# Performance work log

Hardware: AMD Instinct MI355X
Metric: run time of the kernel (lower is better)

Reference implementation:

```python
import jax, jax.numpy as jnp
import numpy as np

EMBED_DIM = 128
TEMP_DIM = EMBED_DIM // 4  # 32
NUM_TYPES = 50
DATE_SCALE = 1825.0
LN_EPS = 1e-5


def _layernorm(x, w, b):
    m = jnp.mean(x, axis=-1, keepdims=True)
    v = jnp.mean((x - m) ** 2, axis=-1, keepdims=True)
    return (x - m) * jax.lax.rsqrt(v + LN_EPS) * w + b


def setup_inputs() -> dict:
    key = jax.random.key(0)
    ks = jax.random.split(key, 16)
    B, L = 4096, 200
    inp = {
        "treatment_ids": jax.random.randint(ks[0], (B, L), 0, NUM_TYPES, dtype=jnp.int64 if jax.config.jax_enable_x64 else jnp.int32),
        "dates": jax.random.uniform(ks[1], (B, L), dtype=jnp.float32) * DATE_SCALE,
        "lengths": jax.random.randint(ks[2], (B,), 0, L + 1, dtype=jnp.int32),
        # parameters
        "emb": jax.random.normal(ks[3], (NUM_TYPES, EMBED_DIM), jnp.float32),
        "tp_w": jax.random.normal(ks[4], (1, TEMP_DIM), jnp.float32) * 0.1,
        "tp_b": jnp.zeros((TEMP_DIM,), jnp.float32),
        "tp_lnw": jnp.ones((TEMP_DIM,), jnp.float32),
        "tp_lnb": jnp.zeros((TEMP_DIM,), jnp.float32),
        "w1": jax.random.normal(ks[5], (EMBED_DIM + TEMP_DIM, EMBED_DIM), jnp.float32) * 0.05,
        "b1": jnp.zeros((EMBED_DIM,), jnp.float32),
        "ln1w": jnp.ones((EMBED_DIM,), jnp.float32),
        "ln1b": jnp.zeros((EMBED_DIM,), jnp.float32),
        "w2": jax.random.normal(ks[6], (EMBED_DIM, EMBED_DIM), jnp.float32) * 0.05,
        "b2": jnp.zeros((EMBED_DIM,), jnp.float32),
        "ln2w": jnp.ones((EMBED_DIM,), jnp.float32),
        "ln2b": jnp.zeros((EMBED_DIM,), jnp.float32),
    }
    return inp


def reference(treatment_ids, dates, lengths, emb, tp_w, tp_b, tp_lnw, tp_lnb,
              w1, b1, ln1w, ln1b, w2, b2, ln2w, ln2b):
    B, L = treatment_ids.shape
    mask = (jnp.arange(L)[None, :] < lengths[:, None]).astype(dates.dtype)  # [B, L]

    # embedding lookup [B, L, D]
    treat = emb[treatment_ids]

    # temporal projection: Linear(1 -> D/4) + LN + GELU
    dn = (dates / DATE_SCALE)[..., None]                      # [B, L, 1]
    temporal = dn * tp_w[0] + tp_b                            # [B, L, D/4]
    temporal = jax.nn.gelu(_layernorm(temporal, tp_lnw, tp_lnb), approximate=False)

    combined = jnp.concatenate([treat, temporal], axis=-1)    # [B, L, D + D/4]

    # sequence encoder (dropout is identity at eval)
    h = jnp.einsum("blk,kd->bld", combined, w1) + b1
    h = jax.nn.gelu(_layernorm(h, ln1w, ln1b), approximate=False)
    h = jnp.einsum("blk,kd->bld", h, w2) + b2
    h = _layernorm(h, ln2w, ln2b)                             # [B, L, D]

    # masked mean pool; empty histories -> zeros
    counts = jnp.sum(mask, axis=1, keepdims=True)             # [B, 1]
    pooled = jnp.sum(h * mask[..., None], axis=1) / jnp.maximum(counts, 1.0)
    return jnp.where(counts > 0, pooled, 0.0)                 # [B, D]
```

## Files before the change

kernel.cpp:

```cpp
#include <hip/hip_runtime.h>
#include <cmath>

#define LN_EPS 1e-5f

typedef float  f32x4  __attribute__((ext_vector_type(4)));
typedef short  short8 __attribute__((ext_vector_type(8)));
typedef unsigned int uint4v __attribute__((ext_vector_type(4)));

#define W1F_U4 2560
#define W2F_U4 2048
#define WLDS_U4 4608

__device__ __forceinline__ unsigned short f32_bf16_rne(float f) {
    union { float f; unsigned u; } v; v.f = f;
    unsigned r = v.u + 0x7FFFu + ((v.u >> 16) & 1u);
    return (unsigned short)(r >> 16);
}

__device__ __forceinline__ unsigned cvt_pk_bf16(float lo, float hi) {
    unsigned r;
    asm("v_cvt_pk_bf16_f32 %0, %1, %2" : "=v"(r) : "v"(lo), "v"(hi));
    return r;
}

__device__ __forceinline__ float gelu_f(float x) {
    float ax = fabsf(x);
    float a  = ax * 0.70710678118654752f;
    float t  = __builtin_amdgcn_rcpf(fmaf(0.3275911f, a, 1.0f));
    float p  = t * fmaf(t, fmaf(t, fmaf(t, fmaf(t, 1.061405429f, -1.453152027f),
                                        1.421413741f), -0.284496736f), 0.254829592f);
    float e  = __builtin_amdgcn_exp2f(-1.44269504089f * a * a);
    float E  = fmaf(-p, e, 1.0f);
    return 0.5f * fmaf(ax, E, x);
}

template<int C>
__device__ __forceinline__ float dpp_radd(float x) {
    int t = __builtin_amdgcn_update_dpp(0, __builtin_bit_cast(int, x), C, 0xF, 0xF, true);
    return x + __builtin_bit_cast(float, t);
}
__device__ __forceinline__ float red16(float x) {
    x = dpp_radd<0x128>(x);
    x = dpp_radd<0x124>(x);
    x = dpp_radd<0x122>(x);
    x = dpp_radd<0x121>(x);
    return x;
}

__global__ void prep_kernel(const float* __restrict__ w1, const float* __restrict__ w2,
                            const float* __restrict__ emb,
                            const float* __restrict__ tp_w, const float* __restrict__ tp_b,
                            unsigned* __restrict__ ws, int emb_pairs) {
    const int tid = blockIdx.x * 256 + threadIdx.x;
    uint4v* w1f = (uint4v*)ws;
    uint4v* w2f = w1f + W1F_U4;
    unsigned* emb16 = (unsigned*)(w2f + W2F_U4);

    for (int i = tid; i < W1F_U4; i += 8192) {
        const int lane = i & 63, nt = (i >> 6) & 7, kt = i >> 9;
        const int k0 = kt * 32 + (lane >> 4) * 8, n = nt * 16 + (lane & 15);
        uint4v r;
        #pragma unroll
        for (int j2 = 0; j2 < 4; ++j2) {
            unsigned lo = f32_bf16_rne(w1[(k0 + 2 * j2) * 128 + n]);
            unsigned hi = f32_bf16_rne(w1[(k0 + 2 * j2 + 1) * 128 + n]);
            r[j2] = lo | (hi << 16);
        }
        w1f[i] = r;
    }
    for (int i = tid; i < W2F_U4; i += 8192) {
        const int lane = i & 63, nt = (i >> 6) & 7, kt = i >> 9;
        const int k0 = kt * 32 + (lane >> 4) * 8, n = nt * 16 + (lane & 15);
        uint4v r;
        #pragma unroll
        for (int j2 = 0; j2 < 4; ++j2) {
            unsigned lo = f32_bf16_rne(w2[(k0 + 2 * j2) * 128 + n]);
            unsigned hi = f32_bf16_rne(w2[(k0 + 2 * j2 + 1) * 128 + n]);
            r[j2] = lo | (hi << 16);
        }
        w2f[i] = r;
    }
    for (int i = tid; i < emb_pairs; i += 8192) {
        unsigned lo = f32_bf16_rne(emb[2 * i]);
        unsigned hi = f32_bf16_rne(emb[2 * i + 1]);
        emb16[i] = lo | (hi << 16);
    }
    if (tid == 0) {
        float Sw = 0.f, Sb = 0.f, Sww = 0.f, Swb = 0.f, Sbb = 0.f;
        for (int j = 0; j < 32; ++j) {
            const float ww = tp_w[j], bb = tp_b[j];
            Sw += ww; Sb += bb; Sww += ww * ww; Swb += ww * bb; Sbb += bb * bb;
        }
        float* tps = (float*)(emb16 + emb_pairs);
        tps[0] = Sw; tps[1] = Sb; tps[2] = Sww; tps[3] = Swb; tps[4] = Sbb;
    }
}

__global__ __launch_bounds__(768, 3) void encoder_mfma(
    const int*   __restrict__ tids,  const float* __restrict__ dates,
    const int*   __restrict__ lengths,
    const float* __restrict__ tp_w,  const float* __restrict__ tp_b,
    const float* __restrict__ tp_lnw,const float* __restrict__ tp_lnb,
    const float* __restrict__ b1,    const float* __restrict__ ln1w, const float* __restrict__ ln1b,
    const float* __restrict__ b2,    const float* __restrict__ ln2w, const float* __restrict__ ln2b,
    const unsigned* __restrict__ ws, float* __restrict__ out,
    int B, int L, int emb_pairs)
{
    __shared__ __align__(16) uint4v wlds[WLDS_U4];
    __shared__ __align__(16) unsigned short a2[12][4][64][8];
    __shared__ float poolbuf[3][4][128];
    __shared__ __align__(16) f32x4 tcoef[32];
    __shared__ __align__(16) f32x4 ecoef1[128];
    __shared__ __align__(16) f32x4 ecoef2[128];

    const int tid = threadIdx.x;
    const int lane = tid & 63, w = tid >> 6;
    const int c = lane & 15, g = lane >> 4;
    const int row = w >> 2, wr = w & 3;
    const int b   = blockIdx.x * 3 + row;

    #pragma unroll
    for (int i = 0; i < 6; ++i)
        wlds[i * 768 + tid] = ((const uint4v*)ws)[i * 768 + tid];

    const unsigned short* emb16 = (const unsigned short*)((const uint4v*)ws + W1F_U4 + W2F_U4);
    const float* tps = (const float*)(emb16 + emb_pairs * 2);

    if (tid < 32)  tcoef[tid]  = (f32x4){tp_w[tid], tp_b[tid], tp_lnw[tid], tp_lnb[tid]};
    if (tid < 128) {
        ecoef1[tid] = (f32x4){b1[tid], ln1w[tid], ln1b[tid], 0.f};
        ecoef2[tid] = (f32x4){b2[tid], ln2w[tid], ln2b[tid], 0.f};
    }
    __syncthreads();

    const float Sw = tps[0], Sb = tps[1], Sww = tps[2], Swb = tps[3], Sbb = tps[4];

    const int len = (b < B) ? min(max(lengths[b], 0), L) : 0;
    const int ntiles = (len + 15) >> 4;

    float pool[8];
    #pragma unroll
    for (int nt = 0; nt < 8; ++nt) pool[nt] = 0.f;
    const int srl = lane ^ ((lane >> 3) & 3);

    for (int t = wr; t < ntiles; t += 4) {
        const int R0 = t << 4;
        const int pc = min(R0 + c, L - 1);
        const int id = tids[b * L + pc];
        const float d = dates[b * L + pc] * (1.f / 1825.f);

        short8 tfrag;
        {
            const float tm = fmaf(d, Sw, Sb) * (1.f / 32.f);
            float tv = fmaf(d * d, Sww, fmaf(2.f * d, Swb, Sbb)) * (1.f / 32.f) - tm * tm;
            const float trs = rsqrtf(fmaxf(tv, 0.f) + LN_EPS);
            const int j0 = g * 8;
            uint4v r;
            #pragma unroll
            for (int j2 = 0; j2 < 4; ++j2) {
                const f32x4 t0 = tcoef[j0 + 2*j2];
                const f32x4 t1 = tcoef[j0 + 2*j2 + 1];
                const float y0 = fmaf((fmaf(d, t0[0], t0[1]) - tm) * trs, t0[2], t0[3]);
                const float y1 = fmaf((fmaf(d, t1[0], t1[1]) - tm) * trs, t1[2], t1[3]);
                r[j2] = cvt_pk_bf16(gelu_f(y0), gelu_f(y1));
            }
            union { uint4v u; short8 s; } cv; cv.u = r;
            tfrag = cv.s;
        }

        f32x4 acc[8];
        #pragma unroll
        for (int nt = 0; nt < 8; ++nt) acc[nt] = (f32x4){0.f, 0.f, 0.f, 0.f};
        __builtin_amdgcn_s_setprio(1);
        #pragma unroll
        for (int kt = 0; kt < 5; ++kt) {
            const short8 af = (kt < 4) ? *(const short8*)(emb16 + id * 128 + kt * 32 + g * 8)
                                       : tfrag;
            #pragma unroll
            for (int nt = 0; nt < 8; ++nt) {
                const short8 bf = ((const short8*)wlds)[(kt * 8 + nt) * 64 + lane];
                acc[nt] = __builtin_amdgcn_mfma_f32_16x16x32_bf16(af, bf, acc[nt], 0, 0, 0);
            }
        }
        __builtin_amdgcn_s_setprio(0);

        {
            f32x4 e1[8];
            #pragma unroll
            for (int nt = 0; nt < 8; ++nt) e1[nt] = ecoef1[nt * 16 + c];
            #pragma unroll
            for (int r = 0; r < 4; ++r) {
                float v[8], s = 0.f, q = 0.f;
                #pragma unroll
                for (int nt = 0; nt < 8; ++nt) {
                    v[nt] = acc[nt][r] + e1[nt][0];
                    s += v[nt]; q = fmaf(v[nt], v[nt], q);
                }
                s = red16(s); q = red16(q);
                const float mean = s * (1.f / 128.f);
                const float var  = fmaxf(q * (1.f / 128.f) - mean * mean, 0.f);
                const float rstd = rsqrtf(var + LN_EPS);
                const int mrow = 4 * g + r;
                #pragma unroll
                for (int n2 = 0; n2 < 4; ++n2) {
                    const float y0 = gelu_f(fmaf((v[2*n2]   - mean) * rstd, e1[2*n2][1],   e1[2*n2][2]));
                    const float y1 = gelu_f(fmaf((v[2*n2+1] - mean) * rstd, e1[2*n2+1][1], e1[2*n2+1][2]));
                    const unsigned pk = cvt_pk_bf16(y0, y1);
                    {
                        const int kcol  = (2*n2) * 16 + c;
                        const int row64 = ((kcol >> 3) & 3) * 16 + mrow;
                        const int srow  = row64 ^ ((row64 >> 3) & 3);
                        a2[w][kcol >> 5][srow][kcol & 7] = (unsigned short)(pk & 0xffffu);
                    }
                    {
                        const int kcol  = (2*n2+1) * 16 + c;
                        const int row64 = ((kcol >> 3) & 3) * 16 + mrow;
                        const int srow  = row64 ^ ((row64 >> 3) & 3);
                        a2[w][kcol >> 5][srow][kcol & 7] = (unsigned short)(pk >> 16);
                    }
                }
            }
        }

        asm volatile("" ::: "memory");

        f32x4 acc2[8];
        #pragma unroll
        for (int nt = 0; nt < 8; ++nt) acc2[nt] = (f32x4){0.f, 0.f, 0.f, 0.f};
        __builtin_amdgcn_s_setprio(1);
        #pragma unroll
        for (int kt2 = 0; kt2 < 4; ++kt2) {
            short8 af;
            __builtin_memcpy(&af, &a2[w][kt2][srl][0], 16);
            #pragma unroll
            for (int nt = 0; nt < 8; ++nt) {
                const short8 bf = ((const short8*)(wlds + W1F_U4))[(kt2 * 8 + nt) * 64 + lane];
                acc2[nt] = __builtin_amdgcn_mfma_f32_16x16x32_bf16(af, bf, acc2[nt], 0, 0, 0);
            }
        }
        __builtin_amdgcn_s_setprio(0);

        asm volatile("" ::: "memory");

        {
            f32x4 e2[8];
            #pragma unroll
            for (int nt = 0; nt < 8; ++nt) e2[nt] = ecoef2[nt * 16 + c];
            #pragma unroll
            for (int r = 0; r < 4; ++r) {
                float v[8], s = 0.f, q = 0.f;
                #pragma unroll
                for (int nt = 0; nt < 8; ++nt) {
                    v[nt] = acc2[nt][r] + e2[nt][0];
                    s += v[nt]; q = fmaf(v[nt], v[nt], q);
                }
                s = red16(s); q = red16(q);
                const float mean = s * (1.f / 128.f);
                const float var  = fmaxf(q * (1.f / 128.f) - mean * mean, 0.f);
                const float rstd = rsqrtf(var + LN_EPS);
                const float msk = ((R0 + 4 * g + r) < len) ? 1.f : 0.f;
                #pragma unroll
                for (int nt = 0; nt < 8; ++nt) {
                    const float y = fmaf((v[nt] - mean) * rstd, e2[nt][1], e2[nt][2]);
                    pool[nt] = fmaf(y, msk, pool[nt]);
                }
            }
        }
    }

    #pragma unroll
    for (int nt = 0; nt < 8; ++nt) {
        float tv = pool[nt];
        tv += __shfl_xor(tv, 16);
        tv += __shfl_xor(tv, 32);
        pool[nt] = tv;
    }
    if (g == 0) {
        #pragma unroll
        for (int nt = 0; nt < 8; ++nt) poolbuf[row][wr][nt * 16 + c] = pool[nt];
    }
    __syncthreads();
    if (tid < 384) {
        const int r3  = tid >> 7;
        const int col = tid & 127;
        const int bo  = blockIdx.x * 3 + r3;
        if (bo < B) {
            const int len2 = min(max(lengths[bo], 0), L);
            const float s = poolbuf[r3][0][col] + poolbuf[r3][1][col]
                          + poolbuf[r3][2][col] + poolbuf[r3][3][col];
            out[bo * 128 + col] = (len2 > 0) ? s / (float)len2 : 0.f;
        }
    }
}

extern "C" void kernel_launch(void* const* d_in, const int* in_sizes, int n_in,
                              void* d_out, int out_size, void* d_ws, size_t ws_size,
                              hipStream_t stream) {
    const int*   tids    = (const int*)  d_in[0];
    const float* dates   = (const float*)d_in[1];
    const int*   lengths = (const int*)  d_in[2];
    const float* emb     = (const float*)d_in[3];
    const float* tp_w    = (const float*)d_in[4];
    const float* tp_b    = (const float*)d_in[5];
    const float* tp_lnw  = (const float*)d_in[6];
    const float* tp_lnb  = (const float*)d_in[7];
    const float* w1      = (const float*)d_in[8];
    const float* b1      = (const float*)d_in[9];
    const float* ln1w    = (const float*)d_in[10];
    const float* ln1b    = (const float*)d_in[11];
    const float* w2      = (const float*)d_in[12];
    const float* b2      = (const float*)d_in[13];
    const float* ln2w    = (const float*)d_in[14];
    const float* ln2b    = (const float*)d_in[15];
    float* out = (float*)d_out;

    const int B = in_sizes[2];
    const int L = in_sizes[0] / B;
    const int emb_pairs = in_sizes[3] / 2;

    hipLaunchKernelGGL(prep_kernel, dim3(32), dim3(256), 0, stream,
                       w1, w2, emb, tp_w, tp_b, (unsigned*)d_ws, emb_pairs);
    hipLaunchKernelGGL(encoder_mfma, dim3((B + 2) / 3), dim3(768), 0, stream,
                       tids, dates, lengths, tp_w, tp_b, tp_lnw, tp_lnb,
                       b1, ln1w, ln1b, b2, ln2w, ln2b,
                       (const unsigned*)d_ws, out, B, L, emb_pairs);
}
```

Before: 214.0 us.

## Precompute embedding-times-W1 table and gather it into accumulators from LDS

Because the embedding lookup is followed by a linear layer, the prep kernel now computes emb·W1[:128] for all 50 types in fp32 and stores the table (padded stride 132). The encoder loads this table into LDS, gathers each row's contribution straight into the MFMA accumulators, and keeps only the temporal K-tile MFMA, cutting the first GEMM from 5 K-steps to 1. The trade-offs are about 26 KB of extra LDS per block, which may lower occupancy, scattered LDS gathers that may cause bank conflicts, and a serial fp32 dot-product loop added to prep. Numerics change slightly since the embedding part is now exact fp32 instead of bf16.

```diff
diff --git a/kernel.cpp b/kernel.cpp
--- a/kernel.cpp
+++ b/kernel.cpp
@@ -7,9 +7,10 @@
 typedef short  short8 __attribute__((ext_vector_type(8)));
 typedef unsigned int uint4v __attribute__((ext_vector_type(4)));
 
-#define W1F_U4 2560
-#define W2F_U4 2048
-#define WLDS_U4 4608
+#define W1TF_U4 512
+#define W2F_U4  2048
+#define E1_U4   1650
+#define WLDS_U4 2560
 
 __device__ __forceinline__ unsigned short f32_bf16_rne(float f) {
     union { float f; unsigned u; } v; v.f = f;
@@ -50,15 +51,16 @@
 __global__ void prep_kernel(const float* __restrict__ w1, const float* __restrict__ w2,
                             const float* __restrict__ emb,
                             const float* __restrict__ tp_w, const float* __restrict__ tp_b,
-                            unsigned* __restrict__ ws, int emb_pairs) {
+                            unsigned* __restrict__ ws) {
     const int tid = blockIdx.x * 256 + threadIdx.x;
-    uint4v* w1f = (uint4v*)ws;
-    uint4v* w2f = w1f + W1F_U4;
-    unsigned* emb16 = (unsigned*)(w2f + W2F_U4);
-
-    for (int i = tid; i < W1F_U4; i += 8192) {
-        const int lane = i & 63, nt = (i >> 6) & 7, kt = i >> 9;
-        const int k0 = kt * 32 + (lane >> 4) * 8, n = nt * 16 + (lane & 15);
+    uint4v* w1tf = (uint4v*)ws;
+    uint4v* w2f  = w1tf + W1TF_U4;
+    float*  E1   = (float*)(w2f + W2F_U4);
+    float*  tps  = E1 + 6600;
+
+    for (int i = tid; i < W1TF_U4; i += 8192) {
+        const int lane = i & 63, nt = i >> 6;
+        const int k0 = 128 + (lane >> 4) * 8, n = nt * 16 + (lane & 15);
         uint4v r;
         #pragma unroll
         for (int j2 = 0; j2 < 4; ++j2) {
@@ -66,7 +68,7 @@
             unsigned hi = f32_bf16_rne(w1[(k0 + 2 * j2 + 1) * 128 + n]);
             r[j2] = lo | (hi << 16);
         }
-        w1f[i] = r;
+        w1tf[i] = r;
     }
     for (int i = tid; i < W2F_U4; i += 8192) {
         const int lane = i & 63, nt = (i >> 6) & 7, kt = i >> 9;
@@ -80,10 +82,12 @@
         }
         w2f[i] = r;
     }
-    for (int i = tid; i < emb_pairs; i += 8192) {
-        unsigned lo = f32_bf16_rne(emb[2 * i]);
-        unsigned hi = f32_bf16_rne(emb[2 * i + 1]);
-        emb16[i] = lo | (hi << 16);
+    if (tid < 6400) {
+        const int t = tid >> 7, n = tid & 127;
+        float s = 0.f;
+        for (int k = 0; k < 128; ++k)
+            s = fmaf(emb[t * 128 + k], w1[k * 128 + n], s);
+        E1[t * 132 + n] = s;
     }
     if (tid == 0) {
         float Sw = 0.f, Sb = 0.f, Sww = 0.f, Swb = 0.f, Sbb = 0.f;
@@ -91,7 +95,6 @@
             const float ww = tp_w[j], bb = tp_b[j];
             Sw += ww; Sb += bb; Sww += ww * ww; Swb += ww * bb; Sbb += bb * bb;
         }
-        float* tps = (float*)(emb16 + emb_pairs);
         tps[0] = Sw; tps[1] = Sb; tps[2] = Sww; tps[3] = Swb; tps[4] = Sbb;
     }
 }
@@ -104,9 +107,10 @@
     const float* __restrict__ b1,    const float* __restrict__ ln1w, const float* __restrict__ ln1b,
     const float* __restrict__ b2,    const float* __restrict__ ln2w, const float* __restrict__ ln2b,
     const unsigned* __restrict__ ws, float* __restrict__ out,
-    int B, int L, int emb_pairs)
+    int B, int L)
 {
     __shared__ __align__(16) uint4v wlds[WLDS_U4];
+    __shared__ __align__(16) float  E1lds[6600];
     __shared__ __align__(16) unsigned short a2[12][4][64][8];
     __shared__ float poolbuf[3][4][128];
     __shared__ __align__(16) f32x4 tcoef[32];
@@ -119,12 +123,12 @@
     const int row = w >> 2, wr = w & 3;
     const int b   = blockIdx.x * 3 + row;
 
-    #pragma unroll
-    for (int i = 0; i < 6; ++i)
-        wlds[i * 768 + tid] = ((const uint4v*)ws)[i * 768 + tid];
-
-    const unsigned short* emb16 = (const unsigned short*)((const uint4v*)ws + W1F_U4 + W2F_U4);
-    const float* tps = (const float*)(emb16 + emb_pairs * 2);
+    for (int i = tid; i < WLDS_U4; i += 768)
+        wlds[i] = ((const uint4v*)ws)[i];
+    for (int i = tid; i < E1_U4; i += 768)
+        ((uint4v*)E1lds)[i] = ((const uint4v*)ws)[WLDS_U4 + i];
+
+    const float* tps = (const float*)((const uint4v*)ws + WLDS_U4 + E1_U4);
 
     if (tid < 32)  tcoef[tid]  = (f32x4){tp_w[tid], tp_b[tid], tp_lnw[tid], tp_lnb[tid]};
     if (tid < 128) {
@@ -146,8 +150,11 @@
     for (int t = wr; t < ntiles; t += 4) {
         const int R0 = t << 4;
         const int pc = min(R0 + c, L - 1);
-        const int id = tids[b * L + pc];
         const float d = dates[b * L + pc] * (1.f / 1825.f);
+        int idr[4];
+        #pragma unroll
+        for (int r = 0; r < 4; ++r)
+            idr[r] = tids[b * L + min(R0 + 4 * g + r, L - 1)];
 
         short8 tfrag;
         {
@@ -170,17 +177,17 @@
 
         f32x4 acc[8];
         #pragma unroll
-        for (int nt = 0; nt < 8; ++nt) acc[nt] = (f32x4){0.f, 0.f, 0.f, 0.f};
+        for (int r = 0; r < 4; ++r) {
+            const int e1base = idr[r] * 132 + c;
+            #pragma unroll
+            for (int nt = 0; nt < 8; ++nt)
+                acc[nt][r] = E1lds[e1base + nt * 16];
+        }
         __builtin_amdgcn_s_setprio(1);
         #pragma unroll
-        for (int kt = 0; kt < 5; ++kt) {
-            const short8 af = (kt < 4) ? *(const short8*)(emb16 + id * 128 + kt * 32 + g * 8)
-                                       : tfrag;
-            #pragma unroll
-            for (int nt = 0; nt < 8; ++nt) {
-                const short8 bf = ((const short8*)wlds)[(kt * 8 + nt) * 64 + lane];
-                acc[nt] = __builtin_amdgcn_mfma_f32_16x16x32_bf16(af, bf, acc[nt], 0, 0, 0);
-            }
+        for (int nt = 0; nt < 8; ++nt) {
+            const short8 bf = ((const short8*)wlds)[nt * 64 + lane];
+            acc[nt] = __builtin_amdgcn_mfma_f32_16x16x32_bf16(tfrag, bf, acc[nt], 0, 0, 0);
         }
         __builtin_amdgcn_s_setprio(0);
 
@@ -234,7 +241,7 @@
             __builtin_memcpy(&af, &a2[w][kt2][srl][0], 16);
             #pragma unroll
             for (int nt = 0; nt < 8; ++nt) {
-                const short8 bf = ((const short8*)(wlds + W1F_U4))[(kt2 * 8 + nt) * 64 + lane];
+                const short8 bf = ((const short8*)(wlds + W1TF_U4))[(kt2 * 8 + nt) * 64 + lane];
                 acc2[nt] = __builtin_amdgcn_mfma_f32_16x16x32_bf16(af, bf, acc2[nt], 0, 0, 0);
             }
         }
@@ -316,12 +323,11 @@
 
     const int B = in_sizes[2];
     const int L = in_sizes[0] / B;
-    const int emb_pairs = in_sizes[3] / 2;
 
     hipLaunchKernelGGL(prep_kernel, dim3(32), dim3(256), 0, stream,
-                       w1, w2, emb, tp_w, tp_b, (unsigned*)d_ws, emb_pairs);
+                       w1, w2, emb, tp_w, tp_b, (unsigned*)d_ws);
     hipLaunchKernelGGL(encoder_mfma, dim3((B + 2) / 3), dim3(768), 0, stream,
                        tids, dates, lengths, tp_w, tp_b, tp_lnw, tp_lnb,
                        b1, ln1w, ln1b, b2, ln2w, ln2b,
-                       (const unsigned*)d_ws, out, B, L, emb_pairs);
-}
+                       (const unsigned*)d_ws, out, B, L);
+}
```

New measurement: 211.5 us. No clear change (-1.2%).
